# Performance work log

Measured on AMD Instinct MI355X. Metric: run time of the kernel, lower is better.

## Reference

```python
import jax, jax.numpy as jnp
import numpy as np

E = 768      # embed_size
H = 12       # num_heads inside each nn.MultiheadAttention
G = 4        # num_groups
D = E // H   # per-head dim = 64


def setup_inputs() -> dict:
    key = jax.random.key(0)
    ks = jax.random.split(key, 20)
    s = 0.02
    B, S = 2, 2048
    inp = {
        "query": jax.random.normal(ks[0], (B, S, E), jnp.float32),
        "key":   jax.random.normal(ks[1], (B, S, E), jnp.float32),
        "value": jax.random.normal(ks[2], (B, S, E), jnp.float32),
        # outer projections (query_group_proj / key_proj / value_proj)
        "Wqg": jax.random.normal(ks[3], (E, E), jnp.float32) * s,
        "bqg": jnp.zeros((E,), jnp.float32),
        "Wk":  jax.random.normal(ks[4], (E, E), jnp.float32) * s,
        "bk":  jnp.zeros((E,), jnp.float32),
        "Wv":  jax.random.normal(ks[5], (E, E), jnp.float32) * s,
        "bv":  jnp.zeros((E,), jnp.float32),
        # per-group MultiheadAttention params (in_proj split into q/k/v, out_proj)
        "Wq_in": jax.random.normal(ks[6], (G, E, E), jnp.float32) * s,
        "bq_in": jnp.zeros((G, E), jnp.float32),
        "Wk_in": jax.random.normal(ks[7], (G, E, E), jnp.float32) * s,
        "bk_in": jnp.zeros((G, E), jnp.float32),
        "Wv_in": jax.random.normal(ks[8], (G, E, E), jnp.float32) * s,
        "bv_in": jnp.zeros((G, E), jnp.float32),
        "Wout":  jax.random.normal(ks[9], (G, E, E), jnp.float32) * s,
        "bout":  jnp.zeros((G, E), jnp.float32),
    }
    return inp


def reference(query, key, value, Wqg, bqg, Wk, bk, Wv, bv,
              Wq_in, bq_in, Wk_in, bk_in, Wv_in, bv_in, Wout, bout):
    B, S, _ = query.shape
    T = S // G  # tokens per group
    scale = 1.0 / np.sqrt(D).astype(np.float32)

    # outer projections (Linear: x @ W.T + b)
    q = query @ Wqg.T + bqg                         # [B,S,E]
    k = key   @ Wk.T  + bk                          # [B,S,E]
    v = value @ Wv.T  + bv                          # [B,S,E]

    # split query tokens into G interleaved groups (view + permute in source)
    qg = q.reshape(B, T, G, E).transpose(0, 2, 1, 3)  # [B,G,T,E]

    # per-group MHA input projections (batched over groups)
    qi = jnp.einsum('bgte,gfe->bgtf', qg, Wq_in) + bq_in[None, :, None, :]
    ki = jnp.einsum('bse,gfe->bgsf', k,  Wk_in) + bk_in[None, :, None, :]
    vi = jnp.einsum('bse,gfe->bgsf', v,  Wv_in) + bv_in[None, :, None, :]

    qh = qi.reshape(B, G, T, H, D)
    kh = ki.reshape(B, G, S, H, D)
    vh = vi.reshape(B, G, S, H, D)

    scores = jnp.einsum('bgthd,bgshd->bghts', qh, kh) * scale  # [B,G,H,T,S]
    attn = jax.nn.softmax(scores, axis=-1)
    ctx = jnp.einsum('bghts,bgshd->bgthd', attn, vh).reshape(B, G, T, E)

    out_g = jnp.einsum('bgte,gfe->bgtf', ctx, Wout) + bout[None, :, None, :]  # [B,G,T,E]

    # reassemble sequence order (inverse of the grouping permutation)
    out = out_g.transpose(0, 2, 1, 3).reshape(B, S, E)
    return out
```

## Files before the change

### kernel.cpp

```cpp
#include <hip/hip_runtime.h>
#include <hip/hip_bf16.h>


typedef __attribute__((ext_vector_type(8))) short short8;
typedef __attribute__((ext_vector_type(4))) float floatx4;
typedef __attribute__((ext_vector_type(4))) int intx4;

static __device__ __forceinline__ short f2bf(float f) {
    __bf16 b = (__bf16)f;
    return __builtin_bit_cast(short, b);
}
static __device__ __forceinline__ short8 f8_to_bf8(floatx4 f0, floatx4 f1) {
    short8 s;
    s[0]=f2bf(f0[0]); s[1]=f2bf(f0[1]); s[2]=f2bf(f0[2]); s[3]=f2bf(f0[3]);
    s[4]=f2bf(f1[0]); s[5]=f2bf(f1[1]); s[6]=f2bf(f1[2]); s[7]=f2bf(f1[3]);
    return s;
}
static __device__ __forceinline__ unsigned cvt_pk_bf16(float a, float b) {
    unsigned r;
    asm("v_cvt_pk_bf16_f32 %0, %1, %2" : "=v"(r) : "v"(a), "v"(b));
    return r;
}
static __device__ __forceinline__ void gload_lds16(const short* g, short* l) {
    __builtin_amdgcn_global_load_lds(
        (const __attribute__((address_space(1))) unsigned int*)g,
        (__attribute__((address_space(3))) unsigned int*)l, 16, 0, 0);
}

__global__ __launch_bounds__(256) void cast_w(
    const float* a0, const float* a1, const float* a2, const float* a3,
    const float* a4, const float* a5, const float* a6, short* dst)
{
    const long U = 589824L;
    const float* ptrs[7] = {a0,a1,a2,a3,a4,a5,a6};
    const long starts[8] = {0, U, 2*U, 3*U, 7*U, 11*U, 15*U, 19*U};
    long i = (long)blockIdx.x * 2048 + (long)threadIdx.x * 8;
    int t = 0;
    while (t < 6 && i >= starts[t + 1]) t++;
    const float* s = ptrs[t] + (i - starts[t]);
    floatx4 f0 = *(const floatx4*)s;
    floatx4 f1 = *(const floatx4*)(s + 4);
    *(short8*)(dst + i) = f8_to_bf8(f0, f1);
}

#define GEMM_LANE_VARS                                                        \
    const int tid = threadIdx.x, lane = tid & 63, w = tid >> 6;               \
    const int wm = w & 1, wn = w >> 1;                                        \
    const int qr = lane >> 4, lc = lane & 15, x7 = lc & 7;                    \
    const int srow = tid >> 3, schunk = tid & 7, sx = srow & 7;

template<int CMODE, int BIAS_MODE>
static __device__ __forceinline__ void gemm_epilogue(
    floatx4 (&acc)[4][4], const float* bp, void* Cv, int ldc, int bm, int bn,
    int wm, int wn, int qr, int lc)
{
#pragma unroll
    for (int ni = 0; ni < 4; ni++) {
        const int gcol = bn * 128 + wn * 64 + ni * 16 + lc;
        const float bcol = (BIAS_MODE == 0) ? bp[gcol] : 0.f;
#pragma unroll
        for (int mi = 0; mi < 4; mi++) {
#pragma unroll
            for (int r = 0; r < 4; r++) {
                const int grow = bm * 128 + wm * 64 + mi * 16 + qr * 4 + r;
                const float bb = (BIAS_MODE == 1) ? bp[grow] : bcol;
                const float v = acc[mi][ni][r] + bb;
                if (CMODE == 0)
                    ((short*)Cv)[(long)grow * ldc + gcol] = f2bf(v);
                else
                    ((float*)Cv)[(long)grow * ldc + gcol] = v;
            }
        }
    }
}

static __device__ __forceinline__ void gemm_mfma_step(
    floatx4 (&acc)[4][4], const short* Ac, const short* Bc,
    int wm, int wn, int qr, int lc, int x7)
{
#pragma unroll
    for (int ks = 0; ks < 64; ks += 32) {
        const int c0 = (ks >> 3) + qr;
        const int slot = ((c0 ^ x7) << 3);
        short8 af[4], bfr[4];
#pragma unroll
        for (int mi = 0; mi < 4; mi++)
            af[mi] = *(const short8*)&Ac[(wm * 64 + mi * 16 + lc) * 64 + slot];
#pragma unroll
        for (int ni = 0; ni < 4; ni++)
            bfr[ni] = *(const short8*)&Bc[(wn * 64 + ni * 16 + lc) * 64 + slot];
#pragma unroll
        for (int mi = 0; mi < 4; mi++)
#pragma unroll
            for (int ni = 0; ni < 4; ni++)
                acc[mi][ni] = __builtin_amdgcn_mfma_f32_16x16x32_bf16(
                    af[mi], bfr[ni], acc[mi][ni], 0, 0, 0);
    }
}

template<int CMODE, int BIAS_MODE>
static __device__ __forceinline__ void gemm_core_db(
    const short* __restrict__ A, const short* __restrict__ Wb,
    const float* __restrict__ bp, void* __restrict__ Cv,
    int lda, int ldc, int bm, int bn, short* As, short* Bs)
{
    GEMM_LANE_VARS
    const short* Ab = A + (long)(bm * 128) * lda;
    const short* Wt = Wb + (long)(bn * 128) * 768;
    const int gch = ((schunk ^ sx) << 3);

    floatx4 acc[4][4];
#pragma unroll
    for (int mi = 0; mi < 4; mi++)
#pragma unroll
        for (int ni = 0; ni < 4; ni++) acc[mi][ni] = (floatx4){0.f, 0.f, 0.f, 0.f};

#pragma unroll
    for (int p = 0; p < 4; p++) {
        gload_lds16(Ab + (long)(p * 32 + srow) * lda + gch, &As[(p * 32 + w * 8) * 64]);
        gload_lds16(Wt + (long)(p * 32 + srow) * 768 + gch, &Bs[(p * 32 + w * 8) * 64]);
    }

    for (int kk = 0; kk < 12; kk++) {
        __syncthreads();
        if (kk < 11) {
            const int k1 = (kk + 1) * 64;
            const int nb = ((kk + 1) & 1) * 8192;
#pragma unroll
            for (int p = 0; p < 4; p++) {
                gload_lds16(Ab + (long)(p * 32 + srow) * lda + k1 + gch,
                            &As[nb + (p * 32 + w * 8) * 64]);
                gload_lds16(Wt + (long)(p * 32 + srow) * 768 + k1 + gch,
                            &Bs[nb + (p * 32 + w * 8) * 64]);
            }
        }
        gemm_mfma_step(acc, As + (kk & 1) * 8192, Bs + (kk & 1) * 8192,
                       wm, wn, qr, lc, x7);
    }
    gemm_epilogue<CMODE, BIAS_MODE>(acc, bp, Cv, ldc, bm, bn, wm, wn, qr, lc);
}

template<int CMODE, int BIAS_MODE>
static __device__ __forceinline__ void gemm_core_f32(
    const float* __restrict__ A, const short* __restrict__ Wb,
    const float* __restrict__ bp, void* __restrict__ Cv,
    int lda, int ldc, int bm, int bn, short* As, short* Bs)
{
    GEMM_LANE_VARS
    const short* Wt = Wb + (long)(bn * 128) * 768;

    floatx4 acc[4][4];
#pragma unroll
    for (int mi = 0; mi < 4; mi++)
#pragma unroll
        for (int ni = 0; ni < 4; ni++) acc[mi][ni] = (floatx4){0.f, 0.f, 0.f, 0.f};

    for (int k0 = 0; k0 < 768; k0 += 64) {
        __syncthreads();
#pragma unroll
        for (int p = 0; p < 4; p++) {
            const int row = p * 32 + srow;
            const float* ap = A + (long)(bm * 128 + row) * lda + k0 + schunk * 8;
            floatx4 f0 = *(const floatx4*)ap;
            floatx4 f1 = *(const floatx4*)(ap + 4);
            *(short8*)&As[row * 64 + ((schunk ^ sx) << 3)] = f8_to_bf8(f0, f1);
            gload_lds16(Wt + (long)row * 768 + k0 + ((schunk ^ sx) << 3),
                        &Bs[(p * 32 + w * 8) * 64]);
        }
        __syncthreads();
        gemm_mfma_step(acc, As, Bs, wm, wn, qr, lc, x7);
    }
    gemm_epilogue<CMODE, BIAS_MODE>(acc, bp, Cv, ldc, bm, bn, wm, wn, qr, lc);
}

__global__ __launch_bounds__(256) void qkv_gemm(
    const float* q, const float* k, const float* v, const short* Wbf,
    const float* bq, const float* bk, const float* bv, short* outp)
{
    __shared__ short As[128 * 64];
    __shared__ short Bs[128 * 64];
    const int xcd = blockIdx.x & 7, slot = blockIdx.x >> 3;
    const int bm = xcd * 4 + slot / 18;
    const int rem = slot % 18, y = rem / 6, bn = rem % 6;
    const float* A    = (y == 0) ? q  : (y == 1) ? k  : v;
    const float* bias = (y == 0) ? bq : (y == 1) ? bk : bv;
    gemm_core_f32<0, 0>(A, Wbf + (long)y * 589824, bias, outp + (long)y * 3145728,
                        768, 768, bm, bn, As, Bs);
}

template<int BIAS_MODE>
static __device__ __forceinline__ void gemm256_core(
    const short* __restrict__ A, const short* __restrict__ B,
    const float* __restrict__ bias, short* __restrict__ C,
    int lda, int ldc, int bm, int bn, short* As, short* Bs)
{
    const int tid = threadIdx.x, lane = tid & 63, w = tid >> 6;
    const int wm = w & 1, wn = w >> 1;
    const int qr = lane >> 4, lc = lane & 15, x7 = lc & 7;
    const int srow = tid >> 3, schunk = tid & 7;
    const int gch = ((schunk ^ (srow & 7)) << 3);

    const short* Ab = A + (long)(bm * 256) * lda;
    const short* Bb = B + (long)(bn * 256) * 768;

    floatx4 acc[8][4];
#pragma unroll
    for (int i = 0; i < 8; i++)
#pragma unroll
        for (int j = 0; j < 4; j++) acc[i][j] = (floatx4){0.f, 0.f, 0.f, 0.f};

#pragma unroll
    for (int r = 0; r < 256; r += 64) {
        gload_lds16(Ab + (long)(r + srow) * lda + gch, As + (r + w * 8) * 64);
        gload_lds16(Bb + (long)(r + srow) * 768 + gch, Bs + (r + w * 8) * 64);
    }

#pragma unroll 1
    for (int kt = 0; kt < 12; ++kt) {
        const int s = kt & 1;
        const short* Ac = As + s * 16384;
        const short* Bc = Bs + s * 16384;
        short* Ad = As + (1 - s) * 16384;
        short* Bd = Bs + (1 - s) * 16384;
        const int koff = (kt + 1) * 64;

        asm volatile("s_waitcnt vmcnt(0)" ::: "memory");
        __builtin_amdgcn_s_barrier();

        short8 af[4][2], bfr[2][2];
#pragma unroll
        for (int ph = 0; ph < 4; ++ph) {
            const int mh = ph >> 1, nh = ph & 1;
            if (nh == 0) {
#pragma unroll
                for (int mi = 0; mi < 4; mi++)
#pragma unroll
                    for (int ks = 0; ks < 2; ks++)
                        af[mi][ks] = *(const short8*)&Ac[
                            (wm * 128 + (mh * 4 + mi) * 16 + lc) * 64 +
                            ((((ks << 2) + qr) ^ x7) << 3)];
            }
#pragma unroll
            for (int ni = 0; ni < 2; ni++)
#pragma unroll
                for (int ks = 0; ks < 2; ks++)
                    bfr[ni][ks] = *(const short8*)&Bc[
                        (wn * 64 + (nh * 2 + ni) * 16 + lc) * 64 +
                        ((((ks << 2) + qr) ^ x7) << 3)];
            if (kt < 11) {
                const int r = ph * 64;
                gload_lds16(Ab + (long)(r + srow) * lda + koff + gch,
                            Ad + (r + w * 8) * 64);
                gload_lds16(Bb + (long)(r + srow) * 768 + koff + gch,
                            Bd + (r + w * 8) * 64);
            }
            __builtin_amdgcn_s_barrier();
            asm volatile("s_waitcnt lgkmcnt(0)" ::: "memory");
            __builtin_amdgcn_sched_barrier(0);
            __builtin_amdgcn_s_setprio(1);
#pragma unroll
            for (int ks = 0; ks < 2; ks++)
#pragma unroll
                for (int mi = 0; mi < 4; mi++)
#pragma unroll
                    for (int ni = 0; ni < 2; ni++)
                        acc[mh * 4 + mi][nh * 2 + ni] =
                            __builtin_amdgcn_mfma_f32_16x16x32_bf16(
                                af[mi][ks], bfr[ni][ks],
                                acc[mh * 4 + mi][nh * 2 + ni], 0, 0, 0);
            __builtin_amdgcn_s_setprio(0);
            __builtin_amdgcn_sched_barrier(0);
            __builtin_amdgcn_s_barrier();
        }
    }

#pragma unroll
    for (int ni = 0; ni < 4; ni++) {
        const int gcol = bn * 256 + wn * 64 + ni * 16 + lc;
        const float bcol = (BIAS_MODE == 0) ? bias[gcol] : 0.f;
#pragma unroll
        for (int mi = 0; mi < 8; mi++) {
#pragma unroll
            for (int r = 0; r < 4; r++) {
                const int grow = bm * 256 + wm * 128 + mi * 16 + qr * 4 + r;
                const float bb = (BIAS_MODE == 1) ? bias[grow] : bcol;
                C[(long)grow * ldc + gcol] = f2bf(acc[mi][ni][r] + bb);
            }
        }
    }
}

__global__ __launch_bounds__(512, 2) void mid_gemm2(
    const short* kproj, const short* vproj, const short* qproj, const short* Wbf,
    const float* bq_in, const float* bk_in, const float* bv_in,
    short* kiB, short* vtB, short* qiB)
{
    __shared__ short As[2 * 16384];
    __shared__ short Bs[2 * 16384];
    const int xcd = blockIdx.x & 7, slot = blockIdx.x >> 3;
    const int z = xcd, b = z >> 2, g = z & 3;
    if (slot < 24) {
        gemm256_core<0>(kproj + (long)b * 1572864, Wbf + (long)(7 + g) * 589824,
                        bk_in + g * 768, kiB + (long)z * 1572864,
                        768, 768, slot / 3, slot % 3, As, Bs);
    } else if (slot < 48) {
        const int s2 = slot - 24;
        gemm256_core<1>(Wbf + (long)(11 + g) * 589824, vproj + (long)b * 1572864,
                        bv_in + g * 768, vtB + (long)z * 1572864,
                        768, 2048, s2 / 8, s2 % 8, As, Bs);
    } else {
        const int s3 = slot - 48;
        gemm256_core<0>(qproj + (long)b * 1572864 + g * 768, Wbf + (long)(3 + g) * 589824,
                        bq_in + g * 768, qiB + (long)z * 393216,
                        3072, 768, s3 / 3, s3 % 3, As, Bs);
    }
}

__global__ __launch_bounds__(256) void out_gemm(
    const short* ctxB, const short* Wbf, const float* bout, float* out)
{
    extern __shared__ short sm[];
    short* As = sm;
    short* Bs = sm + 16384;
    const int xcd = blockIdx.x & 7, slot = blockIdx.x >> 3;
    const int z = xcd, b = z >> 2, g = z & 3;
    gemm_core_db<2, 0>(ctxB + (long)z * 393216, Wbf + (long)(15 + g) * 589824,
                       bout + g * 768, out + (long)b * 1572864 + g * 768,
                       768, 3072, slot / 6, slot % 6, As, Bs);
}

__global__ __launch_bounds__(128) void attn_kernel(
    const short* __restrict__ qi, const short* __restrict__ ki,
    const short* __restrict__ vt, short* __restrict__ ctx)
{
    __shared__ short Kt[2][64 * 64];
    __shared__ short Vt[2][64 * 64];

    const int tid = threadIdx.x, lane = tid & 63, w = tid >> 6;
    const int qr = lane >> 4, lc = lane & 15, x7 = lc & 7;
    const int headid = blockIdx.x % 96;
    const int tile = blockIdx.x / 96;
    const int h = headid % 12, bg = headid / 12;
    const long qrow0 = (long)bg * 512 + tile * 64 + w * 32;

    short8 aq[2][2];
#pragma unroll
    for (int t = 0; t < 2; t++) {
        const short* qp = qi + (qrow0 + t * 16 + lc) * 768 + h * 64 + qr * 8;
        aq[t][0] = *(const short8*)qp;
        aq[t][1] = *(const short8*)(qp + 32);
    }

    floatx4 cacc[2][4];
    float lsum[2] = {0.f, 0.f};
#pragma unroll
    for (int t = 0; t < 2; t++)
#pragma unroll
        for (int dc = 0; dc < 4; dc++) cacc[t][dc] = (floatx4){0.f, 0.f, 0.f, 0.f};

    const int srow = lane >> 3, schk = lane & 7, swz = schk ^ srow;
    const short* kgb = ki + ((long)bg * 2048) * 768 + h * 64;
    const short* vgb = vt + ((long)(bg * 768 + h * 64)) * 2048;

#define KPERM(d) ((((d) >> 5) & 1) * 32 + (((d) >> 2) & 3) * 8 + (((d) >> 4) & 1) * 4 + ((d) & 3))
    int kp[4], dv[4];
#pragma unroll
    for (int inst = 0; inst < 4; inst++) {
        dv[inst] = w * 32 + inst * 8 + srow;
        kp[inst] = KPERM(dv[inst]);
    }
#undef KPERM

    {
#pragma unroll
        for (int inst = 0; inst < 4; inst++) {
            gload_lds16(kgb + (long)kp[inst] * 768 + swz * 8,
                        &Kt[0][(w * 32 + inst * 8) * 64]);
            gload_lds16(vgb + (long)dv[inst] * 2048 + swz * 8,
                        &Vt[0][(w * 32 + inst * 8) * 64]);
        }
    }

    for (int it = 0; it < 32; it++) {
        const int cur = it & 1;
        __syncthreads();
        if (it < 31) {
            const int nxt = cur ^ 1, s0 = (it + 1) * 64;
#pragma unroll
            for (int inst = 0; inst < 4; inst++) {
                gload_lds16(kgb + (long)(s0 + kp[inst]) * 768 + swz * 8,
                            &Kt[nxt][(w * 32 + inst * 8) * 64]);
                gload_lds16(vgb + (long)dv[inst] * 2048 + s0 + swz * 8,
                            &Vt[nxt][(w * 32 + inst * 8) * 64]);
            }
        }

        const short* Kb = &Kt[cur][0];
        const short* Vb = &Vt[cur][0];

        floatx4 sv[2][4];
        __builtin_amdgcn_s_setprio(1);
#pragma unroll
        for (int ss = 0; ss < 4; ss++) {
            const short* kr = Kb + (ss * 16 + lc) * 64;
            short8 b0 = *(const short8*)(kr + ((qr ^ x7) << 3));
            short8 b1 = *(const short8*)(kr + (((4 + qr) ^ x7) << 3));
#pragma unroll
            for (int t = 0; t < 2; t++) {
                floatx4 acc0 = (floatx4){0.f, 0.f, 0.f, 0.f};
                acc0 = __builtin_amdgcn_mfma_f32_16x16x32_bf16(b0, aq[t][0], acc0, 0, 0, 0);
                acc0 = __builtin_amdgcn_mfma_f32_16x16x32_bf16(b1, aq[t][1], acc0, 0, 0, 0);
                sv[t][ss] = acc0;
            }
        }
        __builtin_amdgcn_s_setprio(0);

        short8 ap[2][2];
#pragma unroll
        for (int t = 0; t < 2; t++) {
            float p[4][4];
#pragma unroll
            for (int ss = 0; ss < 4; ss++)
#pragma unroll
                for (int r = 0; r < 4; r++)
                    p[ss][r] = __builtin_amdgcn_exp2f(sv[t][ss][r] * 0.18033688f);
#pragma unroll
            for (int ss = 0; ss < 4; ss++)
                lsum[t] += (p[ss][0] + p[ss][1]) + (p[ss][2] + p[ss][3]);
            intx4 i0, i1;
            i0[0] = (int)cvt_pk_bf16(p[0][0], p[0][1]);
            i0[1] = (int)cvt_pk_bf16(p[0][2], p[0][3]);
            i0[2] = (int)cvt_pk_bf16(p[1][0], p[1][1]);
            i0[3] = (int)cvt_pk_bf16(p[1][2], p[1][3]);
            i1[0] = (int)cvt_pk_bf16(p[2][0], p[2][1]);
            i1[1] = (int)cvt_pk_bf16(p[2][2], p[2][3]);
            i1[2] = (int)cvt_pk_bf16(p[3][0], p[3][1]);
            i1[3] = (int)cvt_pk_bf16(p[3][2], p[3][3]);
            ap[t][0] = __builtin_bit_cast(short8, i0);
            ap[t][1] = __builtin_bit_cast(short8, i1);
        }

        __builtin_amdgcn_s_setprio(1);
#pragma unroll
        for (int dc = 0; dc < 4; dc++) {
            const short* vr = Vb + (dc * 16 + lc) * 64;
            short8 bv0 = *(const short8*)(vr + ((qr ^ x7) << 3));
            short8 bv1 = *(const short8*)(vr + (((4 + qr) ^ x7) << 3));
#pragma unroll
            for (int t = 0; t < 2; t++) {
                cacc[t][dc] = __builtin_amdgcn_mfma_f32_16x16x32_bf16(
                    ap[t][0], bv0, cacc[t][dc], 0, 0, 0);
                cacc[t][dc] = __builtin_amdgcn_mfma_f32_16x16x32_bf16(
                    ap[t][1], bv1, cacc[t][dc], 0, 0, 0);
            }
        }
        __builtin_amdgcn_s_setprio(0);
    }

#pragma unroll
    for (int t = 0; t < 2; t++) {
        lsum[t] += __shfl_xor(lsum[t], 16);
        lsum[t] += __shfl_xor(lsum[t], 32);
    }
    short* cp = ctx + (qrow0)*768 + h * 64;
#pragma unroll
    for (int t = 0; t < 2; t++) {
#pragma unroll
        for (int r = 0; r < 4; r++) {
            const float linv = 1.f / __shfl(lsum[t], qr * 4 + r);
#pragma unroll
            for (int dc = 0; dc < 4; dc++)
                cp[(t * 16 + qr * 4 + r) * 768 + dc * 16 + lc] =
                    f2bf(cacc[t][dc][r] * linv);
        }
    }
}

extern "C" void kernel_launch(void* const* d_in, const int* in_sizes, int n_in,
                              void* d_out, int out_size, void* d_ws, size_t ws_size,
                              hipStream_t stream) {
    const float* query = (const float*)d_in[0];
    const float* key   = (const float*)d_in[1];
    const float* value = (const float*)d_in[2];
    const float* Wqg = (const float*)d_in[3];  const float* bqg = (const float*)d_in[4];
    const float* Wk  = (const float*)d_in[5];  const float* bk  = (const float*)d_in[6];
    const float* Wv  = (const float*)d_in[7];  const float* bv  = (const float*)d_in[8];
    const float* Wq_in = (const float*)d_in[9];  const float* bq_in = (const float*)d_in[10];
    const float* Wk_in = (const float*)d_in[11]; const float* bk_in = (const float*)d_in[12];
    const float* Wv_in = (const float*)d_in[13]; const float* bv_in = (const float*)d_in[14];
    const float* Wout  = (const float*)d_in[15]; const float* bout  = (const float*)d_in[16];
    float* out = (float*)d_out;

    short* ws     = (short*)d_ws;
    short* Wbf    = ws;
    short* q_proj = ws + 11206656L;
    short* k_proj = ws + 14352384L;
    short* v_proj = ws + 17498112L;
    short* qiB    = ws + 20643840L;
    short* vtB    = ws + 23789568L;
    short* kiB    = ws + 36372480L;
    short* ctxB   = ws + 11206656L;

    dim3 blk(256);

    cast_w<<<dim3(5472), blk, 0, stream>>>(
        Wqg, Wk, Wv, Wq_in, Wk_in, Wv_in, Wout, Wbf);

    qkv_gemm<<<dim3(576), blk, 0, stream>>>(
        query, key, value, Wbf, bqg, bk, bv, q_proj);

    mid_gemm2<<<dim3(432), dim3(512), 0, stream>>>(
        k_proj, v_proj, q_proj, Wbf, bq_in, bk_in, bv_in, kiB, vtB, qiB);

    attn_kernel<<<dim3(768), dim3(128), 0, stream>>>(qiB, kiB, vtB, ctxB);

    out_gemm<<<dim3(192), blk, 65536, stream>>>(ctxB, Wbf, bout, out);
}
```

Before: 303.0 us.

## Split attention KV range in two and merge fp32 partials inside output GEMM

```diff
diff --git a/kernel.cpp b/kernel.cpp
--- a/kernel.cpp
+++ b/kernel.cpp
@@ -96,48 +96,6 @@
                 acc[mi][ni] = __builtin_amdgcn_mfma_f32_16x16x32_bf16(
                     af[mi], bfr[ni], acc[mi][ni], 0, 0, 0);
     }
-}
-
-template<int CMODE, int BIAS_MODE>
-static __device__ __forceinline__ void gemm_core_db(
-    const short* __restrict__ A, const short* __restrict__ Wb,
-    const float* __restrict__ bp, void* __restrict__ Cv,
-    int lda, int ldc, int bm, int bn, short* As, short* Bs)
-{
-    GEMM_LANE_VARS
-    const short* Ab = A + (long)(bm * 128) * lda;
-    const short* Wt = Wb + (long)(bn * 128) * 768;
-    const int gch = ((schunk ^ sx) << 3);
-
-    floatx4 acc[4][4];
-#pragma unroll
-    for (int mi = 0; mi < 4; mi++)
-#pragma unroll
-        for (int ni = 0; ni < 4; ni++) acc[mi][ni] = (floatx4){0.f, 0.f, 0.f, 0.f};
-
-#pragma unroll
-    for (int p = 0; p < 4; p++) {
-        gload_lds16(Ab + (long)(p * 32 + srow) * lda + gch, &As[(p * 32 + w * 8) * 64]);
-        gload_lds16(Wt + (long)(p * 32 + srow) * 768 + gch, &Bs[(p * 32 + w * 8) * 64]);
-    }
-
-    for (int kk = 0; kk < 12; kk++) {
-        __syncthreads();
-        if (kk < 11) {
-            const int k1 = (kk + 1) * 64;
-            const int nb = ((kk + 1) & 1) * 8192;
-#pragma unroll
-            for (int p = 0; p < 4; p++) {
-                gload_lds16(Ab + (long)(p * 32 + srow) * lda + k1 + gch,
-                            &As[nb + (p * 32 + w * 8) * 64]);
-                gload_lds16(Wt + (long)(p * 32 + srow) * 768 + k1 + gch,
-                            &Bs[nb + (p * 32 + w * 8) * 64]);
-            }
-        }
-        gemm_mfma_step(acc, As + (kk & 1) * 8192, Bs + (kk & 1) * 8192,
-                       wm, wn, qr, lc, x7);
-    }
-    gemm_epilogue<CMODE, BIAS_MODE>(acc, bp, Cv, ldc, bm, bn, wm, wn, qr, lc);
 }
 
 template<int CMODE, int BIAS_MODE>
@@ -316,22 +274,66 @@
     }
 }
 
+static __device__ __forceinline__ void gemm_core_out(
+    const float* __restrict__ P0, const float* __restrict__ P1,
+    const float* __restrict__ L0, const float* __restrict__ L1,
+    const short* __restrict__ Wb, const float* __restrict__ bp,
+    float* __restrict__ Cv, int z, int bm, int bn, short* As, short* Bs)
+{
+    GEMM_LANE_VARS
+    const short* Wt = Wb + (long)(bn * 128) * 768;
+
+    floatx4 acc[4][4];
+#pragma unroll
+    for (int mi = 0; mi < 4; mi++)
+#pragma unroll
+        for (int ni = 0; ni < 4; ni++) acc[mi][ni] = (floatx4){0.f, 0.f, 0.f, 0.f};
+
+    for (int k0 = 0; k0 < 768; k0 += 64) {
+        __syncthreads();
+        const int e = k0 + schunk * 8, he = e >> 6;
+#pragma unroll
+        for (int p = 0; p < 4; p++) {
+            const int row = p * 32 + srow;
+            const long gz = (long)z * 512 + bm * 128 + row;
+            const float* a0 = P0 + gz * 768 + e;
+            const float* a1 = P1 + gz * 768 + e;
+            floatx4 f0 = *(const floatx4*)a0;
+            floatx4 f1 = *(const floatx4*)(a0 + 4);
+            floatx4 g0 = *(const floatx4*)a1;
+            floatx4 g1 = *(const floatx4*)(a1 + 4);
+            const float linv = 1.f / (L0[gz * 12 + he] + L1[gz * 12 + he]);
+            f0 = (f0 + g0) * linv;
+            f1 = (f1 + g1) * linv;
+            *(short8*)&As[row * 64 + ((schunk ^ sx) << 3)] = f8_to_bf8(f0, f1);
+            gload_lds16(Wt + (long)row * 768 + k0 + ((schunk ^ sx) << 3),
+                        &Bs[(p * 32 + w * 8) * 64]);
+        }
+        __syncthreads();
+        gemm_mfma_step(acc, As, Bs, wm, wn, qr, lc, x7);
+    }
+    gemm_epilogue<2, 0>(acc, bp, Cv, 3072, bm, bn, wm, wn, qr, lc);
+}
+
 __global__ __launch_bounds__(256) void out_gemm(
-    const short* ctxB, const short* Wbf, const float* bout, float* out)
+    const float* P0, const float* P1, const float* L0, const float* L1,
+    const short* Wbf, const float* bout, float* out)
 {
     extern __shared__ short sm[];
     short* As = sm;
     short* Bs = sm + 16384;
     const int xcd = blockIdx.x & 7, slot = blockIdx.x >> 3;
     const int z = xcd, b = z >> 2, g = z & 3;
-    gemm_core_db<2, 0>(ctxB + (long)z * 393216, Wbf + (long)(15 + g) * 589824,
-                       bout + g * 768, out + (long)b * 1572864 + g * 768,
-                       768, 3072, slot / 6, slot % 6, As, Bs);
-}
-
-__global__ __launch_bounds__(128) void attn_kernel(
+    gemm_core_out(P0, P1, L0, L1, Wbf + (long)(15 + g) * 589824,
+                  bout + g * 768, out + (long)b * 1572864 + g * 768,
+                  z, slot / 6, slot % 6, As, Bs);
+}
+
+__global__ __launch_bounds__(256) void attn_kernel(
     const short* __restrict__ qi, const short* __restrict__ ki,
-    const short* __restrict__ vt, short* __restrict__ ctx)
+    const short* __restrict__ vt,
+    float* __restrict__ P0, float* __restrict__ P1,
+    float* __restrict__ L0, float* __restrict__ L1)
 {
     __shared__ short Kt[2][64 * 64];
     __shared__ short Vt[2][64 * 64];
@@ -339,9 +341,11 @@
     const int tid = threadIdx.x, lane = tid & 63, w = tid >> 6;
     const int qr = lane >> 4, lc = lane & 15, x7 = lc & 7;
     const int headid = blockIdx.x % 96;
-    const int tile = blockIdx.x / 96;
+    const int qk = blockIdx.x / 96;
+    const int qt = qk >> 1, kh = qk & 1;
     const int h = headid % 12, bg = headid / 12;
-    const long qrow0 = (long)bg * 512 + tile * 64 + w * 32;
+    const long qrow0 = (long)bg * 512 + qt * 128 + w * 32;
+    const int kbase = kh * 16;
 
     short8 aq[2][2];
 #pragma unroll
@@ -363,36 +367,27 @@
     const short* vgb = vt + ((long)(bg * 768 + h * 64)) * 2048;
 
 #define KPERM(d) ((((d) >> 5) & 1) * 32 + (((d) >> 2) & 3) * 8 + (((d) >> 4) & 1) * 4 + ((d) & 3))
-    int kp[4], dv[4];
-#pragma unroll
-    for (int inst = 0; inst < 4; inst++) {
-        dv[inst] = w * 32 + inst * 8 + srow;
-        kp[inst] = KPERM(dv[inst]);
-    }
+    const int d0 = w * 16 + srow, d1 = d0 + 8;
+    const int kp0 = KPERM(d0), kp1 = KPERM(d1);
 #undef KPERM
 
     {
-#pragma unroll
-        for (int inst = 0; inst < 4; inst++) {
-            gload_lds16(kgb + (long)kp[inst] * 768 + swz * 8,
-                        &Kt[0][(w * 32 + inst * 8) * 64]);
-            gload_lds16(vgb + (long)dv[inst] * 2048 + swz * 8,
-                        &Vt[0][(w * 32 + inst * 8) * 64]);
-        }
-    }
-
-    for (int it = 0; it < 32; it++) {
-        const int cur = it & 1;
+        const int s0 = kbase * 64;
+        gload_lds16(kgb + (long)(s0 + kp0) * 768 + swz * 8, &Kt[0][(w * 16) * 64]);
+        gload_lds16(kgb + (long)(s0 + kp1) * 768 + swz * 8, &Kt[0][(w * 16 + 8) * 64]);
+        gload_lds16(vgb + (long)d0 * 2048 + s0 + swz * 8, &Vt[0][(w * 16) * 64]);
+        gload_lds16(vgb + (long)d1 * 2048 + s0 + swz * 8, &Vt[0][(w * 16 + 8) * 64]);
+    }
+
+    for (int j = 0; j < 16; j++) {
+        const int cur = j & 1;
         __syncthreads();
-        if (it < 31) {
-            const int nxt = cur ^ 1, s0 = (it + 1) * 64;
-#pragma unroll
-            for (int inst = 0; inst < 4; inst++) {
-                gload_lds16(kgb + (long)(s0 + kp[inst]) * 768 + swz * 8,
-                            &Kt[nxt][(w * 32 + inst * 8) * 64]);
-                gload_lds16(vgb + (long)dv[inst] * 2048 + s0 + swz * 8,
-                            &Vt[nxt][(w * 32 + inst * 8) * 64]);
-            }
+        if (j < 15) {
+            const int nxt = cur ^ 1, s0 = (kbase + j + 1) * 64;
+            gload_lds16(kgb + (long)(s0 + kp0) * 768 + swz * 8, &Kt[nxt][(w * 16) * 64]);
+            gload_lds16(kgb + (long)(s0 + kp1) * 768 + swz * 8, &Kt[nxt][(w * 16 + 8) * 64]);
+            gload_lds16(vgb + (long)d0 * 2048 + s0 + swz * 8, &Vt[nxt][(w * 16) * 64]);
+            gload_lds16(vgb + (long)d1 * 2048 + s0 + swz * 8, &Vt[nxt][(w * 16 + 8) * 64]);
         }
 
         const short* Kb = &Kt[cur][0];
@@ -462,17 +457,19 @@
         lsum[t] += __shfl_xor(lsum[t], 16);
         lsum[t] += __shfl_xor(lsum[t], 32);
     }
-    short* cp = ctx + (qrow0)*768 + h * 64;
+
+    float* Pk = kh ? P1 : P0;
+    float* Lk = kh ? L1 : L0;
+    float* cp = Pk + qrow0 * 768 + h * 64;
 #pragma unroll
     for (int t = 0; t < 2; t++) {
 #pragma unroll
-        for (int r = 0; r < 4; r++) {
-            const float linv = 1.f / __shfl(lsum[t], qr * 4 + r);
-#pragma unroll
-            for (int dc = 0; dc < 4; dc++)
-                cp[(t * 16 + qr * 4 + r) * 768 + dc * 16 + lc] =
-                    f2bf(cacc[t][dc][r] * linv);
-        }
+        for (int dc = 0; dc < 4; dc++)
+#pragma unroll
+            for (int r = 0; r < 4; r++)
+                cp[(t * 16 + qr * 4 + r) * 768 + dc * 16 + lc] = cacc[t][dc][r];
+        if (qr == 0)
+            Lk[(qrow0 + t * 16 + lc) * 12 + h] = lsum[t];
     }
 }
 
@@ -499,7 +496,10 @@
     short* qiB    = ws + 20643840L;
     short* vtB    = ws + 23789568L;
     short* kiB    = ws + 36372480L;
-    short* ctxB   = ws + 11206656L;
+    float* P0 = (float*)ws;
+    float* P1 = (float*)(ws + 11206656L);
+    float* L0 = (float*)(ws + 17498112L);
+    float* L1 = (float*)(ws + 17596416L);
 
     dim3 blk(256);
 
@@ -512,7 +512,7 @@
     mid_gemm2<<<dim3(432), dim3(512), 0, stream>>>(
         k_proj, v_proj, q_proj, Wbf, bq_in, bk_in, bv_in, kiB, vtB, qiB);
 
-    attn_kernel<<<dim3(768), dim3(128), 0, stream>>>(qiB, kiB, vtB, ctxB);
-
-    out_gemm<<<dim3(192), blk, 65536, stream>>>(ctxB, Wbf, bout, out);
-}
+    attn_kernel<<<dim3(768), blk, 0, stream>>>(qiB, kiB, vtB, P0, P1, L0, L1);
+
+    out_gemm<<<dim3(192), blk, 65536, stream>>>(P0, P1, L0, L1, Wbf, bout, out);
+}
```

After: 311.7 us. 1.03x slower.
